# Performance work log

Measured on AMD Instinct MI355X. Metric: run time of the kernel, lower is better.

Reference implementation:

```python
import jax, jax.numpy as jnp
import numpy as np
from jax.scipy.special import gammaln

B = 16384
MAX_Y = 4096  # targets drawn from [0, 4096), so k ranges over 0..4095 (covers y.max())
EPS = 1e-6


def setup_inputs() -> dict:
    key = jax.random.key(0)
    k1, k2, k3 = jax.random.split(key, 3)
    r = jax.random.uniform(k1, (B, 2), dtype=jnp.float32) * 20.0 + 0.1  # NB total_count
    p = jax.random.normal(k2, (B, 2), dtype=jnp.float32)
    target = jax.random.randint(k3, (B, 2), 0, MAX_Y, dtype=jnp.int64)
    return {"r": r, "p": p, "target": target}


def _nb_logpmf(k, r, p):
    # torch NegativeBinomial(total_count=r, probs=p).log_prob(k)
    # = lgamma(k+r) - lgamma(k+1) - lgamma(r) + r*log(1-p) + k*log(p)
    return (gammaln(k + r) - gammaln(k + 1.0) - gammaln(r)
            + r * jnp.log1p(-p) + k * jnp.log(p))


def _nb_cdf_bruteforce(y, r, p):
    # brute-force: materialize (B, MAX_Y) log-PMF matrix, mask k<=y, sum
    k = jnp.arange(MAX_Y, dtype=jnp.float32)  # (K,)
    logpmf = _nb_logpmf(k[None, :], r[:, None], p[:, None])  # (B, K)
    mask = k[None, :] <= y[:, None]
    return jnp.sum(jnp.exp(logpmf) * mask, axis=1)


def reference(r, p, target):
    rho = jax.nn.relu(p[:, 1]) + 1.0
    r = jnp.clip(r, 0.0001, None)
    p1 = jnp.clip(jnp.tanh(p[:, 0]), 0.0001, 0.9999)
    y1 = target[:, 0].astype(jnp.float32)
    y2 = target[:, 1].astype(jnp.float32)
    r1, r2 = r[:, 0], r[:, 1]

    logp1 = _nb_logpmf(y1, r1, p1)
    logp2 = _nb_logpmf(y2, r2, p1)  # module reuses p1 for both marginals

    u1 = jnp.clip(_nb_cdf_bruteforce(y1, r1, p1), EPS, 1.0 - EPS)
    u2 = jnp.clip(_nb_cdf_bruteforce(y2, r2, p1), EPS, 1.0 - EPS)

    theta = jnp.maximum(rho, 1.00001)
    t1 = (-jnp.log(u1)) ** theta
    t2 = (-jnp.log(u2)) ** theta
    # original computes log(exp(-(t1+t2)**(1/theta))) — kept faithful
    logc = jnp.log(jnp.exp(-((t1 + t2) ** (1.0 / theta))))

    ll = logp1 + logp2 + logc
    return -jnp.mean(ll)
```

## Files before the change

### kernel.cpp

```cpp
#include <hip/hip_runtime.h>
#include <math.h>

#define NROWS 16384

__device__ __forceinline__ float prod8(float x) {
    return ((x * (x + 1.f)) * ((x + 2.f) * (x + 3.f))) *
           (((x + 4.f) * (x + 5.f)) * ((x + 6.f) * (x + 7.f)));
}

__device__ __forceinline__ float lgam(float x) {
    float z  = x + 8.f;
    float lz = __logf(z);
    float zi = __builtin_amdgcn_rcpf(z);
    return (z - 0.5f) * lz - z + 0.91893853f + 0.08333333f * zi - __logf(prod8(x));
}

__device__ __forceinline__ float lgam_diff(float a, float b) {
    float za = a + 8.f, zb = b + 8.f;
    float la = __logf(za), lb = __logf(zb);
    float ra = __builtin_amdgcn_rcpf(za), rb = __builtin_amdgcn_rcpf(zb);
    return (za - 0.5f) * la - (zb - 0.5f) * lb - (a - b)
         + 0.08333333f * (ra - rb)
         + __logf(prod8(b) * __builtin_amdgcn_rcpf(prod8(a)));
}

__global__ __launch_bounds__(256) void nb_rows(
    const float* __restrict__ r,
    const float* __restrict__ p,
    const int*   __restrict__ tg,
    float* __restrict__ ws,
    float* __restrict__ out)
{
    __shared__ float su[4], sv[4];
    const int tid  = threadIdx.x;
    const int w    = tid >> 6;
    const int lane = tid & 63;
    const int rm   = blockIdx.x * 4 + w;
    const int row  = rm >> 1;
    const int j    = rm & 1;

    const float rr = fmaxf(r[2 * row + j], 1e-4f);
    const float p0 = p[2 * row];
    const float e2 = __expf(2.f * p0);
    const float p1 = fminf(fmaxf(1.f - 2.f * __builtin_amdgcn_rcpf(e2 + 1.f), 1e-4f), 0.9999f);
    const int   y  = tg[2 * row + j];
    const float yf = (float)y;

    const float q1   = 1.f - p1;
    const float logp = __logf(p1);
    const float base = rr * __logf(q1) - lgam(rr);

    const float qi = __builtin_amdgcn_rcpf(q1);
    const float rp = rr * p1;
    const int   K  = (int)fminf(fmaf(6.f, __fsqrt_rn(rp) * qi, rp * qi) + 16.f, yf);

    const int c = (K + 64) >> 6;
    const int s = lane * c;
    float acc = 0.f;
    if (s <= K) {
        const int   cnt = min(c, K + 1 - s);
        const float sf  = (float)s;
        float pmf = __expf(lgam_diff(sf + rr, sf + 1.f) + base + sf * logp);
        acc = pmf;
        float kf = sf + 1.f;
        float pk = p1 * (sf + rr);
        for (int m = 1; m < cnt; ++m) {
            pmf *= pk * __builtin_amdgcn_rcpf(kf);
            acc += pmf;
            pk += p1;
            kf += 1.f;
        }
    }
    #pragma unroll
    for (int off = 32; off; off >>= 1) acc += __shfl_xor(acc, off);

    const float lpy = lgam_diff(yf + rr, yf + 1.f) + base + yf * logp;

    if (lane == 0) {
        su[w] = fminf(fmaxf(acc, 1e-6f), 1.f - 1e-6f);
        sv[w] = lpy;
    }
    __syncthreads();
    if (tid < 2) {
        const int   rrow  = blockIdx.x * 2 + tid;
        const float u1    = su[2 * tid], u2 = su[2 * tid + 1];
        const float theta = fmaxf(fmaxf(p[2 * rrow + 1], 0.f) + 1.f, 1.00001f);
        const float x1 = -__logf(u1);
        const float x2 = -__logf(u2);
        const float t1 = __expf(theta * __logf(x1));
        const float t2 = __expf(theta * __logf(x2));
        const float logc = -__expf(__logf(t1 + t2) * __builtin_amdgcn_rcpf(theta));
        const float nll  = -(sv[2 * tid] + sv[2 * tid + 1] + logc);
        if (ws) ws[rrow] = nll;
        else    atomicAdd(out, nll * (1.f / (float)NROWS));
    }
}

__global__ __launch_bounds__(1024) void reduce_ws(
    const float* __restrict__ ws, float* __restrict__ out)
{
    __shared__ float sm[16];
    const int t = threadIdx.x;
    float a0 = 0.f, a1 = 0.f, a2 = 0.f, a3 = 0.f;
    #pragma unroll
    for (int i = 0; i < 4; ++i) {
        const int b = t + i * 4096;
        a0 += ws[b];
        a1 += ws[b + 1024];
        a2 += ws[b + 2048];
        a3 += ws[b + 3072];
    }
    float a = (a0 + a1) + (a2 + a3);
    #pragma unroll
    for (int off = 32; off; off >>= 1) a += __shfl_xor(a, off);
    if ((t & 63) == 0) sm[t >> 6] = a;
    __syncthreads();
    if (t < 16) {
        float b = sm[t];
        b += __shfl_xor(b, 1);
        b += __shfl_xor(b, 2);
        b += __shfl_xor(b, 4);
        b += __shfl_xor(b, 8);
        if (t == 0) out[0] = b * (1.f / (float)NROWS);
    }
}

extern "C" void kernel_launch(void* const* d_in, const int* in_sizes, int n_in,
                              void* d_out, int out_size, void* d_ws, size_t ws_size,
                              hipStream_t stream) {
    const float* r  = (const float*)d_in[0];
    const float* p  = (const float*)d_in[1];
    const int*   tg = (const int*)d_in[2];
    float* out = (float*)d_out;

    if (ws_size >= NROWS * sizeof(float)) {
        float* ws = (float*)d_ws;
        nb_rows<<<2 * NROWS / 4, 256, 0, stream>>>(r, p, tg, ws, nullptr);
        reduce_ws<<<1, 1024, 0, stream>>>(ws, out);
    } else {
        hipMemsetAsync(out, 0, sizeof(float), stream);
        nb_rows<<<2 * NROWS / 4, 256, 0, stream>>>(r, p, tg, nullptr, out);
    }
}
```

Baseline: 76.14 us.

## Process four marginals per wave with half-wave splits and DPP reductions

Each wave now handles two rows (four marginals), with each half-wave summing one marginal's CDF over 32-lane chunks, and two independent marginals interleaved in one loop for ILP. Cross-lane sums use DPP row operations instead of shuffles, and the copula is computed in-register per wave, so each block writes one partial sum and the final reducer reads only 2048 values. This halves the grid and cuts the per-row workspace traffic, but doubles the per-lane serial chain length and adds divergence when the two marginals have different term counts. The fallback path for a small workspace is removed.

```diff
diff --git a/kernel.cpp b/kernel.cpp
--- a/kernel.cpp
+++ b/kernel.cpp
@@ -24,93 +24,125 @@
          + __logf(prod8(b) * __builtin_amdgcn_rcpf(prod8(a)));
 }
 
+template <int CTRL>
+__device__ __forceinline__ float dpp_add(float v) {
+    int t = __builtin_amdgcn_update_dpp(0, __float_as_int(v), CTRL, 0xf, 0xf, true);
+    return v + __int_as_float(t);
+}
+__device__ __forceinline__ float half_reduce(float v) {
+    v = dpp_add<0x111>(v);
+    v = dpp_add<0x112>(v);
+    v = dpp_add<0x114>(v);
+    v = dpp_add<0x118>(v);
+    v = dpp_add<0x142>(v);
+    return v;
+}
+
+__device__ __forceinline__ float copula_nll(float u1, float u2, float th,
+                                            float lp1, float lp2) {
+    const float theta = fmaxf(fmaxf(th, 0.f) + 1.f, 1.00001f);
+    const float x1 = -__logf(u1);
+    const float x2 = -__logf(u2);
+    const float t1 = __expf(theta * __logf(x1));
+    const float t2 = __expf(theta * __logf(x2));
+    const float logc = -__expf(__logf(t1 + t2) * __builtin_amdgcn_rcpf(theta));
+    return -(lp1 + lp2 + logc);
+}
+
 __global__ __launch_bounds__(256) void nb_rows(
     const float* __restrict__ r,
     const float* __restrict__ p,
     const int*   __restrict__ tg,
-    float* __restrict__ ws,
-    float* __restrict__ out)
+    float* __restrict__ partial)
 {
-    __shared__ float su[4], sv[4];
+    __shared__ float sb[4];
     const int tid  = threadIdx.x;
     const int w    = tid >> 6;
     const int lane = tid & 63;
-    const int rm   = blockIdx.x * 4 + w;
-    const int row  = rm >> 1;
-    const int j    = rm & 1;
+    const int wid  = blockIdx.x * 4 + w;
+    const int j    = lane >> 5;
+    const int sl   = lane & 31;
+    const int b4   = 4 * wid;
 
-    const float rr = fmaxf(r[2 * row + j], 1e-4f);
-    const float p0 = p[2 * row];
-    const float e2 = __expf(2.f * p0);
-    const float p1 = fminf(fmaxf(1.f - 2.f * __builtin_amdgcn_rcpf(e2 + 1.f), 1e-4f), 0.9999f);
-    const int   y  = tg[2 * row + j];
-    const float yf = (float)y;
+    const float rA  = fmaxf(r[b4 + j], 1e-4f);
+    const float rB  = fmaxf(r[b4 + 2 + j], 1e-4f);
+    const float p0A = p[b4],     p0B = p[b4 + 2];
+    const float thA = p[b4 + 1], thB = p[b4 + 3];
+    const int   yA  = tg[b4 + j], yB = tg[b4 + 2 + j];
+    const float yAf = (float)yA,  yBf = (float)yB;
 
-    const float q1   = 1.f - p1;
-    const float logp = __logf(p1);
-    const float base = rr * __logf(q1) - lgam(rr);
+    const float e2A = __expf(2.f * p0A), e2B = __expf(2.f * p0B);
+    const float p1A = fminf(fmaxf(1.f - 2.f * __builtin_amdgcn_rcpf(e2A + 1.f), 1e-4f), 0.9999f);
+    const float p1B = fminf(fmaxf(1.f - 2.f * __builtin_amdgcn_rcpf(e2B + 1.f), 1e-4f), 0.9999f);
+    const float qA  = 1.f - p1A,  qB  = 1.f - p1B;
+    const float lpA = __logf(p1A), lpB = __logf(p1B);
+    const float baseA = rA * __logf(qA) - lgam(rA);
+    const float baseB = rB * __logf(qB) - lgam(rB);
 
-    const float qi = __builtin_amdgcn_rcpf(q1);
-    const float rp = rr * p1;
-    const int   K  = (int)fminf(fmaf(6.f, __fsqrt_rn(rp) * qi, rp * qi) + 16.f, yf);
+    const float qiA = __builtin_amdgcn_rcpf(qA), qiB = __builtin_amdgcn_rcpf(qB);
+    const float rpA = rA * p1A, rpB = rB * p1B;
+    const int KA = (int)fminf(fmaf(6.f, __fsqrt_rn(rpA) * qiA, rpA * qiA) + 16.f, yAf);
+    const int KB = (int)fminf(fmaf(6.f, __fsqrt_rn(rpB) * qiB, rpB * qiB) + 16.f, yBf);
 
-    const int c = (K + 64) >> 6;
-    const int s = lane * c;
-    float acc = 0.f;
-    if (s <= K) {
-        const int   cnt = min(c, K + 1 - s);
-        const float sf  = (float)s;
-        float pmf = __expf(lgam_diff(sf + rr, sf + 1.f) + base + sf * logp);
-        acc = pmf;
-        float kf = sf + 1.f;
-        float pk = p1 * (sf + rr);
-        for (int m = 1; m < cnt; ++m) {
-            pmf *= pk * __builtin_amdgcn_rcpf(kf);
-            acc += pmf;
-            pk += p1;
-            kf += 1.f;
+    const int cA = (KA + 32) >> 5, cB = (KB + 32) >> 5;
+    const int sA = sl * cA,        sB = sl * cB;
+
+    float accA = 0.f, pmfA = 0.f, kfA = 0.f, pkA = 0.f;
+    float accB = 0.f, pmfB = 0.f, kfB = 0.f, pkB = 0.f;
+    int cntA = 0, cntB = 0;
+    if (sA <= KA) {
+        cntA = min(cA, KA + 1 - sA);
+        const float sf = (float)sA;
+        pmfA = __expf(lgam_diff(sf + rA, sf + 1.f) + baseA + sf * lpA);
+        accA = pmfA;  kfA = sf + 1.f;  pkA = p1A * (sf + rA);
+    }
+    if (sB <= KB) {
+        cntB = min(cB, KB + 1 - sB);
+        const float sf = (float)sB;
+        pmfB = __expf(lgam_diff(sf + rB, sf + 1.f) + baseB + sf * lpB);
+        accB = pmfB;  kfB = sf + 1.f;  pkB = p1B * (sf + rB);
+    }
+
+    const int mmax = max(cntA, cntB);
+    for (int m = 1; m < mmax; ++m) {
+        if (m < cntA) {
+            pmfA *= pkA * __builtin_amdgcn_rcpf(kfA);
+            accA += pmfA;  pkA += p1A;  kfA += 1.f;
+        }
+        if (m < cntB) {
+            pmfB *= pkB * __builtin_amdgcn_rcpf(kfB);
+            accB += pmfB;  pkB += p1B;  kfB += 1.f;
         }
     }
-    #pragma unroll
-    for (int off = 32; off; off >>= 1) acc += __shfl_xor(acc, off);
 
-    const float lpy = lgam_diff(yf + rr, yf + 1.f) + base + yf * logp;
+    float uA = half_reduce(accA);
+    float uB = half_reduce(accB);
+    uA = fminf(fmaxf(uA, 1e-6f), 1.f - 1e-6f);
+    uB = fminf(fmaxf(uB, 1e-6f), 1.f - 1e-6f);
 
-    if (lane == 0) {
-        su[w] = fminf(fmaxf(acc, 1e-6f), 1.f - 1e-6f);
-        sv[w] = lpy;
+    const float lpyA = lgam_diff(yAf + rA, yAf + 1.f) + baseA + yAf * lpA;
+    const float lpyB = lgam_diff(yBf + rB, yBf + 1.f) + baseB + yBf * lpB;
+
+    const float uAo   = __shfl_xor(uA, 32);
+    const float uBo   = __shfl_xor(uB, 32);
+    const float lpyAo = __shfl_xor(lpyA, 32);
+    const float lpyBo = __shfl_xor(lpyB, 32);
+
+    if (lane == 31) {
+        sb[w] = copula_nll(uA, uAo, thA, lpyA, lpyAo)
+              + copula_nll(uB, uBo, thB, lpyB, lpyBo);
     }
     __syncthreads();
-    if (tid < 2) {
-        const int   rrow  = blockIdx.x * 2 + tid;
-        const float u1    = su[2 * tid], u2 = su[2 * tid + 1];
-        const float theta = fmaxf(fmaxf(p[2 * rrow + 1], 0.f) + 1.f, 1.00001f);
-        const float x1 = -__logf(u1);
-        const float x2 = -__logf(u2);
-        const float t1 = __expf(theta * __logf(x1));
-        const float t2 = __expf(theta * __logf(x2));
-        const float logc = -__expf(__logf(t1 + t2) * __builtin_amdgcn_rcpf(theta));
-        const float nll  = -(sv[2 * tid] + sv[2 * tid + 1] + logc);
-        if (ws) ws[rrow] = nll;
-        else    atomicAdd(out, nll * (1.f / (float)NROWS));
-    }
+    if (tid == 0)
+        partial[blockIdx.x] = (sb[0] + sb[1]) + (sb[2] + sb[3]);
 }
 
-__global__ __launch_bounds__(1024) void reduce_ws(
-    const float* __restrict__ ws, float* __restrict__ out)
+__global__ __launch_bounds__(1024) void reduce_p(
+    const float* __restrict__ pp, float* __restrict__ out)
 {
     __shared__ float sm[16];
     const int t = threadIdx.x;
-    float a0 = 0.f, a1 = 0.f, a2 = 0.f, a3 = 0.f;
-    #pragma unroll
-    for (int i = 0; i < 4; ++i) {
-        const int b = t + i * 4096;
-        a0 += ws[b];
-        a1 += ws[b + 1024];
-        a2 += ws[b + 2048];
-        a3 += ws[b + 3072];
-    }
-    float a = (a0 + a1) + (a2 + a3);
+    float a = pp[t] + pp[t + 1024];
     #pragma unroll
     for (int off = 32; off; off >>= 1) a += __shfl_xor(a, off);
     if ((t & 63) == 0) sm[t >> 6] = a;
@@ -132,13 +164,8 @@
     const float* p  = (const float*)d_in[1];
     const int*   tg = (const int*)d_in[2];
     float* out = (float*)d_out;
+    float* partial = (float*)d_ws;
 
-    if (ws_size >= NROWS * sizeof(float)) {
-        float* ws = (float*)d_ws;
-        nb_rows<<<2 * NROWS / 4, 256, 0, stream>>>(r, p, tg, ws, nullptr);
-        reduce_ws<<<1, 1024, 0, stream>>>(ws, out);
-    } else {
-        hipMemsetAsync(out, 0, sizeof(float), stream);
-        nb_rows<<<2 * NROWS / 4, 256, 0, stream>>>(r, p, tg, nullptr, out);
-    }
+    nb_rows<<<2048, 256, 0, stream>>>(r, p, tg, partial);
+    reduce_p<<<1, 1024, 0, stream>>>(partial, out);
 }
```

After: 76.74 us. Within noise of the previous version (+0.8%).
